# Kernel optimization log

Measured on AMD Instinct MI355X. Metric: run time of the kernel, lower is better.

## Reference

```python
import jax, jax.numpy as jnp
import numpy as np
from jax import lax

EPS = 1e-12


def _l2norm(v):
    return v / (jnp.sqrt(jnp.sum(v * v)) + EPS)


def _spectral_norm(W, u):
    # one torch-style power iteration; u, v are treated as constants
    v = lax.stop_gradient(_l2norm(W.T @ u))
    u2 = lax.stop_gradient(_l2norm(W @ v))
    sigma = u2 @ (W @ v)
    return W / sigma


def _lstm(gates_x, Whh):
    # gates_x: [B, T, 4H] = x @ Wih^T + b_ih + b_hh, precomputed
    B, T, G = gates_x.shape
    H = G // 4
    WhhT = Whh.T  # [H, 4H]

    def step(carry, gx_t):
        h, c = carry
        gates = gx_t + h @ WhhT  # [B, 4H]
        i = jax.nn.sigmoid(gates[:, 0 * H:1 * H])
        f = jax.nn.sigmoid(gates[:, 1 * H:2 * H])
        g = jnp.tanh(gates[:, 2 * H:3 * H])
        o = jax.nn.sigmoid(gates[:, 3 * H:4 * H])
        c = f * c + i * g
        h = o * jnp.tanh(c)
        return (h, c), h

    h0 = jnp.zeros((B, H), gates_x.dtype)
    c0 = jnp.zeros((B, H), gates_x.dtype)
    _, hs = lax.scan(step, (h0, c0), jnp.swapaxes(gates_x, 0, 1))
    return jnp.swapaxes(hs, 0, 1)  # [B, T, H]


def setup_inputs() -> dict:
    key = jax.random.key(0)
    ks = jax.random.split(key, 8)
    B, T, C, H = 512, 512, 32, 128
    Cin = C + 1  # minibatch-std channel
    init = lambda k, shp: 0.02 * jax.random.normal(k, shp, dtype=jnp.float32)
    return {
        "x": jax.random.normal(ks[0], (B, T, C), dtype=jnp.float32),
        "w_ih_orig": init(ks[1], (4 * H, Cin)),
        "u_ih": _l2norm(jax.random.normal(ks[2], (4 * H,), dtype=jnp.float32)),
        "w_hh_orig": init(ks[3], (4 * H, H)),
        "u_hh": _l2norm(jax.random.normal(ks[4], (4 * H,), dtype=jnp.float32)),
        "b_ih": jnp.zeros((4 * H,), jnp.float32),
        "b_hh": jnp.zeros((4 * H,), jnp.float32),
        "attn_w": init(ks[5], (1, H)),
        "attn_b": jnp.zeros((1,), jnp.float32),
        "fc_w_orig": init(ks[6], (1, H)),
        "u_fc": _l2norm(jax.random.normal(ks[7], (1,), dtype=jnp.float32)),
        "fc_b": jnp.zeros((1,), jnp.float32),
    }


def reference(x, w_ih_orig, u_ih, w_hh_orig, u_hh, b_ih, b_hh,
              attn_w, attn_b, fc_w_orig, u_fc, fc_b):
    B = x.shape[0]
    # minibatch std feature (torch std: unbiased, ddof=1)
    std_per_step = jnp.std(x, axis=0, ddof=1, keepdims=True)        # [1,T,C]
    std_scalar = jnp.mean(std_per_step, axis=-1, keepdims=True)     # [1,T,1]
    std_channel = jnp.broadcast_to(std_scalar, (B,) + std_scalar.shape[1:])
    x = jnp.concatenate([x, std_channel], axis=-1)                  # [B,T,C+1]

    Wih = _spectral_norm(w_ih_orig, u_ih)
    Whh = _spectral_norm(w_hh_orig, u_hh)
    gates_x = jnp.einsum("btc,gc->btg", x, Wih) + b_ih + b_hh       # [B,T,4H]
    h = _lstm(gates_x, Whh)                                          # [B,T,H]

    attn_logits = jnp.einsum("bth,oh->bto", h, attn_w) + attn_b     # [B,T,1]
    attn = jax.nn.softmax(attn_logits, axis=1)
    pooled = jnp.sum(attn * h, axis=1)                               # [B,H]

    Wfc = _spectral_norm(fc_w_orig, u_fc)
    score = pooled @ Wfc.T + fc_b                                    # [B,1]
    return score
```

## Files before the change

kernel.cpp:

```cpp
#include <hip/hip_runtime.h>
#include <math.h>

#define TT 512
#define BB 512
#define CC 32
#define CIN 33
#define HH 128
#define EPSF 1e-12f
#define CH 16
#define NCH (TT / CH)
#define RB 2
#define HSP 160
#define XSP 96

typedef _Float16 half8 __attribute__((ext_vector_type(8)));
typedef _Float16 half4v __attribute__((ext_vector_type(4)));
typedef _Float16 half2v __attribute__((ext_vector_type(2)));
typedef float f32x4 __attribute__((ext_vector_type(4)));

#define MFMA16H(a, b, c) __builtin_amdgcn_mfma_f32_16x16x32_f16(a, b, c, 0, 0, 0)

__device__ __forceinline__ float fsig(float x) {
    return __builtin_amdgcn_rcpf(1.f + __expf(-x));
}
__device__ __forceinline__ float ftanh(float x) {
    return 1.f - 2.f * __builtin_amdgcn_rcpf(1.f + __expf(2.f * x));
}
__device__ __forceinline__ float wave_sum_dpp(float x) {
    x += __int_as_float(__builtin_amdgcn_update_dpp(0, __float_as_int(x), 0x111, 0xf, 0xf, true));
    x += __int_as_float(__builtin_amdgcn_update_dpp(0, __float_as_int(x), 0x112, 0xf, 0xf, true));
    x += __int_as_float(__builtin_amdgcn_update_dpp(0, __float_as_int(x), 0x114, 0xf, 0xf, true));
    x += __int_as_float(__builtin_amdgcn_update_dpp(0, __float_as_int(x), 0x118, 0xf, 0xf, true));
    x += __int_as_float(__builtin_amdgcn_update_dpp(0, __float_as_int(x), 0x142, 0xa, 0xf, true));
    x += __int_as_float(__builtin_amdgcn_update_dpp(0, __float_as_int(x), 0x143, 0xc, 0xf, true));
    return x;
}
__device__ __forceinline__ float row_sum_dpp(float x) {
    x += __int_as_float(__builtin_amdgcn_update_dpp(0, __float_as_int(x), 0x111, 0xf, 0xf, true));
    x += __int_as_float(__builtin_amdgcn_update_dpp(0, __float_as_int(x), 0x112, 0xf, 0xf, true));
    x += __int_as_float(__builtin_amdgcn_update_dpp(0, __float_as_int(x), 0x114, 0xf, 0xf, true));
    x += __int_as_float(__builtin_amdgcn_update_dpp(0, __float_as_int(x), 0x118, 0xf, 0xf, true));
    return x;
}
__device__ __forceinline__ float load_s(const float* p) {
    float v = __hip_atomic_load(p, __ATOMIC_RELAXED, __HIP_MEMORY_SCOPE_AGENT);
    for (int it = 0; it < 100000000 && __float_as_uint(v) == 0xAAAAAAAAu; ++it)
        v = __hip_atomic_load(p, __ATOMIC_RELAXED, __HIP_MEMORY_SCOPE_AGENT);
    return v;
}

__global__ __attribute__((amdgpu_flat_work_group_size(512, 512), amdgpu_waves_per_eu(2, 2)))
void critic_fused(
    const float* __restrict__ x,
    const float* __restrict__ w_ih, const float* __restrict__ u_ih,
    const float* __restrict__ w_hh, const float* __restrict__ u_hh,
    const float* __restrict__ b_ih, const float* __restrict__ b_hh,
    const float* __restrict__ attn_w, const float* __restrict__ attn_b,
    const float* __restrict__ fc_w, const float* __restrict__ u_fc,
    const float* __restrict__ fc_b,
    float* __restrict__ ws,
    float* __restrict__ out)
{
    const int tid = threadIdx.x;
    const int w   = tid >> 6;
    const int l   = tid & 63;
    const int m   = l & 15;
    const int q   = l >> 4;
    const int r   = q & 1;
    const int b0  = blockIdx.x * RB;
    const int jcol = 16 * w + m;

    __shared__ float4 sSS[2][8][8];
    __shared__ float4 sQQ[2][8][8];
    __shared__ float stdp[2][8];
    __shared__ float red[512];
    __shared__ float vv[128];
    __shared__ float sigS[3];
    __shared__ __align__(16) _Float16 hs[2][RB][HSP];
    __shared__ __align__(16) _Float16 xs[2][CH][RB][XSP];
    __shared__ float ss[2][CH];
    __shared__ __align__(8) float bcast[2][RB];
    __shared__ float Sf[RB];
    __shared__ float part[8][RB];

    const int c4 = tid & 7;
    const int bs = tid >> 3;
    float4 xa[2][8];
#pragma unroll
    for (int tt = 0; tt < 2; ++tt) {
        const int t = 2 * blockIdx.x + tt;
#pragma unroll
        for (int i = 0; i < 8; ++i)
            xa[tt][i] = *reinterpret_cast<const float4*>(
                x + ((size_t)(bs * 8 + i) * TT + t) * CC + c4 * 4);
    }

    {
        const int c = tid & 127, qq = tid >> 7;
        const float* wp = w_hh + (size_t)(qq * 128) * HH + c;
        const float* up = u_hh + qq * 128;
        float a0 = 0.f, a1 = 0.f, a2 = 0.f, a3 = 0.f;
#pragma unroll 4
        for (int g = 0; g < 128; g += 4) {
            a0 = fmaf(wp[(size_t)(g + 0) * HH], up[g + 0], a0);
            a1 = fmaf(wp[(size_t)(g + 1) * HH], up[g + 1], a1);
            a2 = fmaf(wp[(size_t)(g + 2) * HH], up[g + 2], a2);
            a3 = fmaf(wp[(size_t)(g + 3) * HH], up[g + 3], a3);
        }
        red[tid] = (a0 + a1) + (a2 + a3);
    }

#pragma unroll
    for (int tt = 0; tt < 2; ++tt) {
        float4 S = make_float4(0.f, 0.f, 0.f, 0.f);
        float4 Q = make_float4(0.f, 0.f, 0.f, 0.f);
#pragma unroll
        for (int i = 0; i < 8; ++i) {
            float4 v = xa[tt][i];
            S.x += v.x; S.y += v.y; S.z += v.z; S.w += v.w;
            Q.x = fmaf(v.x, v.x, Q.x); Q.y = fmaf(v.y, v.y, Q.y);
            Q.z = fmaf(v.z, v.z, Q.z); Q.w = fmaf(v.w, v.w, Q.w);
        }
#pragma unroll
        for (int off = 8; off <= 32; off <<= 1) {
            S.x += __shfl_xor(S.x, off, 64); S.y += __shfl_xor(S.y, off, 64);
            S.z += __shfl_xor(S.z, off, 64); S.w += __shfl_xor(S.w, off, 64);
            Q.x += __shfl_xor(Q.x, off, 64); Q.y += __shfl_xor(Q.y, off, 64);
            Q.z += __shfl_xor(Q.z, off, 64); Q.w += __shfl_xor(Q.w, off, 64);
        }
        if (l < 8) { sSS[tt][w][c4] = S; sQQ[tt][w][c4] = Q; }
    }
    __syncthreads();

    if (tid < 128) vv[tid] = red[tid] + red[tid + 128] + red[tid + 256] + red[tid + 384];
    if (tid >= 384 && tid < 400) {
        const int tt2 = (tid - 384) >> 3, cc = (tid - 384) & 7;
        float4 St = make_float4(0.f, 0.f, 0.f, 0.f);
        float4 Qt = make_float4(0.f, 0.f, 0.f, 0.f);
#pragma unroll
        for (int i = 0; i < 8; ++i) {
            float4 a = sSS[tt2][i][cc], b4 = sQQ[tt2][i][cc];
            St.x += a.x; St.y += a.y; St.z += a.z; St.w += a.w;
            Qt.x += b4.x; Qt.y += b4.y; Qt.z += b4.z; Qt.w += b4.w;
        }
        float st = 0.f;
#pragma unroll
        for (int i = 0; i < 4; ++i) {
            float s1 = (i == 0) ? St.x : (i == 1) ? St.y : (i == 2) ? St.z : St.w;
            float q1 = (i == 0) ? Qt.x : (i == 1) ? Qt.y : (i == 2) ? Qt.z : Qt.w;
            float mean = s1 / 512.0f;
            float var  = (q1 - 512.0f * mean * mean) / 511.0f;
            st += sqrtf(fmaxf(var, 0.f));
        }
        stdp[tt2][cc] = st;
    }
    __syncthreads();
    if (tid >= 408 && tid < 410) {
        const int tt2 = tid - 408;
        float mm = 0.f;
#pragma unroll
        for (int i = 0; i < 8; ++i) mm += stdp[tt2][i];
        __hip_atomic_store(&ws[2 * blockIdx.x + tt2], mm / 32.0f, __ATOMIC_RELAXED,
                           __HIP_MEMORY_SCOPE_AGENT);
    }
    red[tid] = (tid < 128) ? vv[tid] * vv[tid] : 0.f;
    __syncthreads();

    {
        for (int s = 64; s >= 1; s >>= 1) { if (tid < s) red[tid] += red[tid + s]; __syncthreads(); }
        const float nv = sqrtf(red[0]);
        __syncthreads();
        if (tid < 128) vv[tid] = vv[tid] / (nv + EPSF);
        __syncthreads();
        float sq = 0.f;
        float2 vl = *reinterpret_cast<const float2*>(&vv[2 * l]);
#pragma unroll 4
        for (int gi = 0; gi < 64; ++gi) {
            const int g = w * 64 + gi;
            float2 wl = *reinterpret_cast<const float2*>(&w_hh[(size_t)g * HH + 2 * l]);
            float p  = fmaf(wl.x, vl.x, wl.y * vl.y);
            float tot = wave_sum_dpp(p);
            sq = fmaf(tot, tot, sq);
        }
        if (l == 63) red[w] = sq;
        __syncthreads();
        if (tid == 0) {
            float ns2 = 0.f;
            for (int i = 0; i < 8; ++i) ns2 += red[i];
            sigS[1] = ns2 / (sqrtf(ns2) + EPSF);
        }
        __syncthreads();
    }
    {
        if (l < CIN) {
            float a0 = 0.f, a1 = 0.f;
#pragma unroll 4
            for (int gi = 0; gi < 64; gi += 2) {
                const int g = w * 64 + gi;
                a0 = fmaf(w_ih[(size_t)(g + 0) * CIN + l], u_ih[g + 0], a0);
                a1 = fmaf(w_ih[(size_t)(g + 1) * CIN + l], u_ih[g + 1], a1);
            }
            red[w * 64 + l] = a0 + a1;
        }
        __syncthreads();
        if (tid < CIN) {
            float v = 0.f;
#pragma unroll
            for (int i = 0; i < 8; ++i) v += red[i * 64 + tid];
            vv[tid] = v;
        }
        __syncthreads();
        if (tid == 0) {
            float n2 = 0.f;
            for (int i = 0; i < CIN; ++i) n2 += vv[i] * vv[i];
            red[400] = sqrtf(n2);
        }
        __syncthreads();
        const float nv = red[400];
        if (tid < CIN) vv[tid] = vv[tid] / (nv + EPSF);
        __syncthreads();
        float vl = (l < CIN) ? vv[l] : 0.f;
        float sq = 0.f;
#pragma unroll 4
        for (int gi = 0; gi < 64; ++gi) {
            const int g = w * 64 + gi;
            float p = (l < CIN) ? w_ih[(size_t)g * CIN + l] * vl : 0.f;
            float tot = wave_sum_dpp(p);
            sq = fmaf(tot, tot, sq);
        }
        if (l == 63) red[w] = sq;
        __syncthreads();
        if (tid == 0) {
            float ns2 = 0.f;
            for (int i = 0; i < 8; ++i) ns2 += red[i];
            sigS[0] = ns2 / (sqrtf(ns2) + EPSF);
        }
        __syncthreads();
    }
    {
        red[tid] = (tid < 128) ? fc_w[tid] * fc_w[tid] : 0.f;
        __syncthreads();
        for (int s = 64; s >= 1; s >>= 1) { if (tid < s) red[tid] += red[tid + s]; __syncthreads(); }
        if (tid == 0) {
            float nw2 = red[0];
            float u0  = u_fc[0];
            float nv  = fabsf(u0) * sqrtf(nw2);
            float wv  = u0 * nw2 / (nv + EPSF);
            sigS[2]   = wv * wv / (fabsf(wv) + EPSF);
        }
        __syncthreads();
    }
    const float rih = 1.f / sigS[0];
    const float rhh = 1.f / sigS[1];
    const float rfc = 1.f / sigS[2];
    const float attb = attn_b[0];

    half8 Bf[4][5];
    float biasg[4], w32g[4];
#pragma unroll
    for (int p = 0; p < 4; ++p) {
        const int g = 16 * w + 128 * p + m;
#pragma unroll
        for (int kt = 0; kt < 4; ++kt) {
            const float* src = w_hh + (size_t)g * HH + kt * 32 + q * 8;
#pragma unroll
            for (int i = 0; i < 8; ++i) Bf[p][kt][i] = (_Float16)(src[i] * rhh);
        }
        {
            const float* src = w_ih + (size_t)g * CIN + q * 8;
#pragma unroll
            for (int i = 0; i < 8; ++i) Bf[p][4][i] = (_Float16)(src[i] * rih);
        }
        w32g[p]  = w_ih[(size_t)g * CIN + 32] * rih;
        biasg[p] = b_ih[g] + b_hh[g];
    }
    f32x4 zero4 = (f32x4){0.f, 0.f, 0.f, 0.f};
#pragma unroll
    for (int p = 0; p < 4; ++p) {
#pragma unroll
        for (int kt = 0; kt < 5; ++kt) asm volatile("" : "+v"(Bf[p][kt]));
        asm volatile("" : "+v"(biasg[p]), "+v"(w32g[p]));
    }
    asm volatile("" : "+v"(zero4));
    const float fcwj = fc_w[jcol] * rfc;
    const float aw0 = attn_w[2 * l];
    const float aw1 = attn_w[2 * l + 1];

    for (int i = tid; i < 2 * RB * HSP; i += 512) (&hs[0][0][0])[i] = (_Float16)0.f;
    if (tid < 256) {
        const int cc4 = tid & 7, rr = (tid >> 3) & 1, k = tid >> 4;
        float4 xv = *reinterpret_cast<const float4*>(x + ((size_t)(b0 + rr) * TT + k) * CC + cc4 * 4);
        half4v hv = {(_Float16)xv.x, (_Float16)xv.y, (_Float16)xv.z, (_Float16)xv.w};
        *(half4v*)&xs[0][k][rr][cc4 * 4] = hv;
    }
    if (tid < CH) ss[0][tid] = load_s(&ws[tid]);

    float c_st = 0.f, P = 0.f, hprev = 0.f, hpp = 0.f;
    float Sreg = 0.f;
    __syncthreads();

    for (int tc = 0; tc < NCH; ++tc) {
        const int cb = tc & 1;

        if (tc + 1 < NCH) {
            const int nb  = (tc + 1) & 1;
            const int t0n = (tc + 1) * CH;
            if (tid < 256) {
                const int cc4 = tid & 7, rr = (tid >> 3) & 1, k = tid >> 4;
                float4 xv = *reinterpret_cast<const float4*>(
                    x + ((size_t)(b0 + rr) * TT + (t0n + k)) * CC + cc4 * 4);
                half4v hv = {(_Float16)xv.x, (_Float16)xv.y, (_Float16)xv.z, (_Float16)xv.w};
                *(half4v*)&xs[nb][k][rr][cc4 * 4] = hv;
            }
            if (tid < CH) ss[nb][tid] = load_s(&ws[t0n + tid]);
        }

        for (int k = 0; k < CH; ++k) {
            const int t  = tc * CH + k;
            const int hb = (t + 1) & 1;

            half8 ah0 = *(const half8*)&hs[hb][m & 1][0 * 32 + q * 8];
            half8 ah1 = *(const half8*)&hs[hb][m & 1][1 * 32 + q * 8];
            half8 ah2 = *(const half8*)&hs[hb][m & 1][2 * 32 + q * 8];
            half8 ah3 = *(const half8*)&hs[hb][m & 1][3 * 32 + q * 8];
            half8 ah4 = *(const half8*)&xs[cb][k][m & 1][q * 8];
            const float s_t = ss[cb][k];

            float dotp = 0.f;
            if (t > 0 && w < RB) {
                half2v hh = *(const half2v*)&hs[hb][w][2 * l];
                dotp = fmaf(aw0, (float)hh[0], aw1 * (float)hh[1]);
            }

            if (t >= 2) P = fmaf(bcast[(t - 1) & 1][r], hpp, P);

            f32x4 acc0 = MFMA16H(ah0, Bf[0][0], zero4);
            f32x4 acc1 = MFMA16H(ah0, Bf[1][0], zero4);
            f32x4 acc2 = MFMA16H(ah0, Bf[2][0], zero4);
            f32x4 acc3 = MFMA16H(ah0, Bf[3][0], zero4);
            acc0 = MFMA16H(ah1, Bf[0][1], acc0);
            acc1 = MFMA16H(ah1, Bf[1][1], acc1);
            acc2 = MFMA16H(ah1, Bf[2][1], acc2);
            acc3 = MFMA16H(ah1, Bf[3][1], acc3);
            acc0 = MFMA16H(ah2, Bf[0][2], acc0);
            acc1 = MFMA16H(ah2, Bf[1][2], acc1);
            acc2 = MFMA16H(ah2, Bf[2][2], acc2);
            acc3 = MFMA16H(ah2, Bf[3][2], acc3);
            acc0 = MFMA16H(ah3, Bf[0][3], acc0);
            acc1 = MFMA16H(ah3, Bf[1][3], acc1);
            acc2 = MFMA16H(ah3, Bf[2][3], acc2);
            acc3 = MFMA16H(ah3, Bf[3][3], acc3);
            acc0 = MFMA16H(ah4, Bf[0][4], acc0);
            acc1 = MFMA16H(ah4, Bf[1][4], acc1);
            acc2 = MFMA16H(ah4, Bf[2][4], acc2);
            acc3 = MFMA16H(ah4, Bf[3][4], acc3);

            if (t > 0 && w < RB) {
                float tot = wave_sum_dpp(dotp);
                if (l == 63) {
                    float beta = __expf(tot + attb);
                    Sreg += beta;
                    bcast[t & 1][w] = beta;
                }
            }

            {
                float g0 = acc0[r] + fmaf(w32g[0], s_t, biasg[0]);
                float g1 = acc1[r] + fmaf(w32g[1], s_t, biasg[1]);
                float g2 = acc2[r] + fmaf(w32g[2], s_t, biasg[2]);
                float g3 = acc3[r] + fmaf(w32g[3], s_t, biasg[3]);
                float ig = fsig(g0);
                float fg = fsig(g1);
                float gg = ftanh(g2);
                float og = fsig(g3);
                c_st = fmaf(fg, c_st, ig * gg);
                float hv = og * ftanh(c_st);
                hpp   = hprev;
                hprev = hv;
                if (q < 2) hs[t & 1][r][jcol] = (_Float16)hv;
            }

            __syncthreads();
        }
    }

    P = fmaf(bcast[1][r], hpp, P);
    if (w < RB) {
        half2v hh = *(const half2v*)&hs[1][w][2 * l];
        float dotp = fmaf(aw0, (float)hh[0], aw1 * (float)hh[1]);
        float tot = wave_sum_dpp(dotp);
        if (l == 63) {
            float beta = __expf(tot + attb);
            Sreg += beta;
            bcast[0][w] = beta;
            Sf[w] = Sreg;
        }
    }
    __syncthreads();
    {
        float Pv = fmaf(bcast[0][r], hprev, P);
        float v  = Pv * __builtin_amdgcn_rcpf(Sf[r]) * fcwj;
        float rs = row_sum_dpp(v);
        if (l == 15) part[w][0] = rs;
        if (l == 31) part[w][1] = rs;
    }
    __syncthreads();
    if (tid < RB) {
        float a = 0.f;
#pragma unroll
        for (int i = 0; i < 8; ++i) a += part[i][tid];
        out[b0 + tid] = a + fc_b[0];
    }
}

extern "C" void kernel_launch(void* const* d_in, const int* in_sizes, int n_in,
                              void* d_out, int out_size, void* d_ws, size_t ws_size,
                              hipStream_t stream) {
    const float* x      = (const float*)d_in[0];
    const float* w_ih   = (const float*)d_in[1];
    const float* u_ih   = (const float*)d_in[2];
    const float* w_hh   = (const float*)d_in[3];
    const float* u_hh   = (const float*)d_in[4];
    const float* b_ih   = (const float*)d_in[5];
    const float* b_hh   = (const float*)d_in[6];
    const float* attn_w = (const float*)d_in[7];
    const float* attn_b = (const float*)d_in[8];
    const float* fc_w   = (const float*)d_in[9];
    const float* u_fc   = (const float*)d_in[10];
    const float* fc_b   = (const float*)d_in[11];
    float* ws  = (float*)d_ws;
    float* out = (float*)d_out;

    critic_fused<<<BB / RB, 512, 0, stream>>>(x, w_ih, u_ih, w_hh, u_hh, b_ih, b_hh,
                                              attn_w, attn_b, fc_w, u_fc, fc_b, ws, out);
}
```

Baseline: 467.4 us.

## Precompute input-gate projections per chunk via MFMA, off the recurrent critical path

The x-projection MFMA (fifth K-slice) leaves the per-step recurrent chain. Instead, the next chunk's gate pre-activations, including the std-channel term and biases, are computed in bulk with MFMAs partway through the current chunk and stored as fp32 in shared memory. Each step then does 16 MFMAs plus four LDS loads. The change also swaps __syncthreads for a raw lgkmcnt wait plus s_barrier, and moves the attention waves to waves 6-7. The cost is a much larger LDS footprint (about 130KB) and extra LDS traffic.

```diff
diff --git a/kernel.cpp b/kernel.cpp
--- a/kernel.cpp
+++ b/kernel.cpp
@@ -11,14 +11,14 @@
 #define NCH (TT / CH)
 #define RB 2
 #define HSP 160
-#define XSP 96
+#define GXP 520
 
 typedef _Float16 half8 __attribute__((ext_vector_type(8)));
-typedef _Float16 half4v __attribute__((ext_vector_type(4)));
 typedef _Float16 half2v __attribute__((ext_vector_type(2)));
 typedef float f32x4 __attribute__((ext_vector_type(4)));
 
 #define MFMA16H(a, b, c) __builtin_amdgcn_mfma_f32_16x16x32_f16(a, b, c, 0, 0, 0)
+#define BARRIER() asm volatile("s_waitcnt lgkmcnt(0)\n\ts_barrier" ::: "memory")
 
 __device__ __forceinline__ float fsig(float x) {
     return __builtin_amdgcn_rcpf(1.f + __expf(-x));
@@ -77,8 +77,7 @@
     __shared__ float vv[128];
     __shared__ float sigS[3];
     __shared__ __align__(16) _Float16 hs[2][RB][HSP];
-    __shared__ __align__(16) _Float16 xs[2][CH][RB][XSP];
-    __shared__ float ss[2][CH];
+    __shared__ float gxs[2][2 * CH][GXP];
     __shared__ __align__(8) float bcast[2][RB];
     __shared__ float Sf[RB];
     __shared__ float part[8][RB];
@@ -286,114 +285,139 @@
     const float aw0 = attn_w[2 * l];
     const float aw1 = attn_w[2 * l + 1];
 
+#define STAGE_LOAD(t0_, xr_)                                                   \
+    {                                                                          \
+        _Pragma("unroll")                                                      \
+        for (int mt = 0; mt < 2; ++mt) {                                       \
+            const size_t base =                                                \
+                ((size_t)(b0 + (m & 1)) * TT + ((t0_) + 8 * mt + (m >> 1))) *  \
+                    CC + q * 8;                                                \
+            xr_[mt][0] = *reinterpret_cast<const float4*>(x + base);           \
+            xr_[mt][1] = *reinterpret_cast<const float4*>(x + base + 4);       \
+        }                                                                      \
+    }
+
+#define STAGE_COMMIT(t0_, nb_, xr_)                                            \
+    {                                                                          \
+        _Pragma("unroll")                                                      \
+        for (int mt = 0; mt < 2; ++mt) {                                       \
+            half8 af = {(_Float16)xr_[mt][0].x, (_Float16)xr_[mt][0].y,        \
+                        (_Float16)xr_[mt][0].z, (_Float16)xr_[mt][0].w,        \
+                        (_Float16)xr_[mt][1].x, (_Float16)xr_[mt][1].y,        \
+                        (_Float16)xr_[mt][1].z, (_Float16)xr_[mt][1].w};       \
+            f32x4 s0 = MFMA16H(af, Bf[0][4], zero4);                           \
+            f32x4 s1 = MFMA16H(af, Bf[1][4], zero4);                           \
+            f32x4 s2 = MFMA16H(af, Bf[2][4], zero4);                           \
+            f32x4 s3 = MFMA16H(af, Bf[3][4], zero4);                           \
+            const float svl = load_s(&ws[(t0_) + 8 * mt + 2 * q]);             \
+            const float svh = load_s(&ws[(t0_) + 8 * mt + 2 * q + 1]);         \
+            const int row0 = 16 * mt + 4 * q;                                  \
+            _Pragma("unroll")                                                  \
+            for (int j = 0; j < 4; ++j) {                                      \
+                const float sv = (j & 2) ? svh : svl;                          \
+                gxs[nb_][row0 + j][jcol + 0]   = s0[j] + fmaf(w32g[0], sv, biasg[0]); \
+                gxs[nb_][row0 + j][jcol + 128] = s1[j] + fmaf(w32g[1], sv, biasg[1]); \
+                gxs[nb_][row0 + j][jcol + 256] = s2[j] + fmaf(w32g[2], sv, biasg[2]); \
+                gxs[nb_][row0 + j][jcol + 384] = s3[j] + fmaf(w32g[3], sv, biasg[3]); \
+            }                                                                  \
+        }                                                                      \
+    }
+
+#define LSTM_STEP(t_, k_, cb_)                                                 \
+    {                                                                          \
+        const int t  = (t_);                                                   \
+        const int hb = (t + 1) & 1;                                            \
+        half8 ah0 = *(const half8*)&hs[hb][m & 1][0 * 32 + q * 8];             \
+        half8 ah1 = *(const half8*)&hs[hb][m & 1][1 * 32 + q * 8];             \
+        half8 ah2 = *(const half8*)&hs[hb][m & 1][2 * 32 + q * 8];             \
+        half8 ah3 = *(const half8*)&hs[hb][m & 1][3 * 32 + q * 8];             \
+        const float* gxr = &gxs[cb_][((k_) << 1) | r][jcol];                   \
+        float gx0 = gxr[0];                                                    \
+        float gx1 = gxr[128];                                                  \
+        float gx2 = gxr[256];                                                  \
+        float gx3 = gxr[384];                                                  \
+        float dotp = 0.f;                                                      \
+        if (t > 0 && w >= 6) {                                                 \
+            half2v hh = *(const half2v*)&hs[hb][w - 6][2 * l];                 \
+            dotp = fmaf(aw0, (float)hh[0], aw1 * (float)hh[1]);                \
+        }                                                                      \
+        if (t >= 2) P = fmaf(bcast[(t - 1) & 1][r], hpp, P);                   \
+        f32x4 acc0 = MFMA16H(ah0, Bf[0][0], zero4);                            \
+        f32x4 acc1 = MFMA16H(ah0, Bf[1][0], zero4);                            \
+        f32x4 acc2 = MFMA16H(ah0, Bf[2][0], zero4);                            \
+        f32x4 acc3 = MFMA16H(ah0, Bf[3][0], zero4);                            \
+        acc0 = MFMA16H(ah1, Bf[0][1], acc0);                                   \
+        acc1 = MFMA16H(ah1, Bf[1][1], acc1);                                   \
+        acc2 = MFMA16H(ah1, Bf[2][1], acc2);                                   \
+        acc3 = MFMA16H(ah1, Bf[3][1], acc3);                                   \
+        acc0 = MFMA16H(ah2, Bf[0][2], acc0);                                   \
+        acc1 = MFMA16H(ah2, Bf[1][2], acc1);                                   \
+        acc2 = MFMA16H(ah2, Bf[2][2], acc2);                                   \
+        acc3 = MFMA16H(ah2, Bf[3][2], acc3);                                   \
+        acc0 = MFMA16H(ah3, Bf[0][3], acc0);                                   \
+        acc1 = MFMA16H(ah3, Bf[1][3], acc1);                                   \
+        acc2 = MFMA16H(ah3, Bf[2][3], acc2);                                   \
+        acc3 = MFMA16H(ah3, Bf[3][3], acc3);                                   \
+        if (t > 0 && w >= 6) {                                                 \
+            float tot = wave_sum_dpp(dotp);                                    \
+            if (l == 63) {                                                     \
+                float beta = __expf(tot + attb);                               \
+                Sreg += beta;                                                  \
+                bcast[t & 1][w - 6] = beta;                                    \
+            }                                                                  \
+        }                                                                      \
+        {                                                                      \
+            float g0 = acc0[r] + gx0;                                          \
+            float g1 = acc1[r] + gx1;                                          \
+            float g2 = acc2[r] + gx2;                                          \
+            float g3 = acc3[r] + gx3;                                          \
+            float ig = fsig(g0);                                               \
+            float fg = fsig(g1);                                               \
+            float gg = ftanh(g2);                                              \
+            float og = fsig(g3);                                               \
+            c_st = fmaf(fg, c_st, ig * gg);                                    \
+            float hv = og * ftanh(c_st);                                       \
+            hpp   = hprev;                                                     \
+            hprev = hv;                                                        \
+            if (q < 2) hs[t & 1][r][jcol] = (_Float16)hv;                      \
+        }                                                                      \
+        BARRIER();                                                             \
+    }
+
     for (int i = tid; i < 2 * RB * HSP; i += 512) (&hs[0][0][0])[i] = (_Float16)0.f;
-    if (tid < 256) {
-        const int cc4 = tid & 7, rr = (tid >> 3) & 1, k = tid >> 4;
-        float4 xv = *reinterpret_cast<const float4*>(x + ((size_t)(b0 + rr) * TT + k) * CC + cc4 * 4);
-        half4v hv = {(_Float16)xv.x, (_Float16)xv.y, (_Float16)xv.z, (_Float16)xv.w};
-        *(half4v*)&xs[0][k][rr][cc4 * 4] = hv;
-    }
-    if (tid < CH) ss[0][tid] = load_s(&ws[tid]);
 
     float c_st = 0.f, P = 0.f, hprev = 0.f, hpp = 0.f;
     float Sreg = 0.f;
+
+    {
+        float4 xr0[2][2];
+        STAGE_LOAD(0, xr0);
+        STAGE_COMMIT(0, 0, xr0);
+    }
     __syncthreads();
 
     for (int tc = 0; tc < NCH; ++tc) {
-        const int cb = tc & 1;
-
-        if (tc + 1 < NCH) {
-            const int nb  = (tc + 1) & 1;
-            const int t0n = (tc + 1) * CH;
-            if (tid < 256) {
-                const int cc4 = tid & 7, rr = (tid >> 3) & 1, k = tid >> 4;
-                float4 xv = *reinterpret_cast<const float4*>(
-                    x + ((size_t)(b0 + rr) * TT + (t0n + k)) * CC + cc4 * 4);
-                half4v hv = {(_Float16)xv.x, (_Float16)xv.y, (_Float16)xv.z, (_Float16)xv.w};
-                *(half4v*)&xs[nb][k][rr][cc4 * 4] = hv;
-            }
-            if (tid < CH) ss[nb][tid] = load_s(&ws[t0n + tid]);
-        }
-
-        for (int k = 0; k < CH; ++k) {
-            const int t  = tc * CH + k;
-            const int hb = (t + 1) & 1;
-
-            half8 ah0 = *(const half8*)&hs[hb][m & 1][0 * 32 + q * 8];
-            half8 ah1 = *(const half8*)&hs[hb][m & 1][1 * 32 + q * 8];
-            half8 ah2 = *(const half8*)&hs[hb][m & 1][2 * 32 + q * 8];
-            half8 ah3 = *(const half8*)&hs[hb][m & 1][3 * 32 + q * 8];
-            half8 ah4 = *(const half8*)&xs[cb][k][m & 1][q * 8];
-            const float s_t = ss[cb][k];
-
-            float dotp = 0.f;
-            if (t > 0 && w < RB) {
-                half2v hh = *(const half2v*)&hs[hb][w][2 * l];
-                dotp = fmaf(aw0, (float)hh[0], aw1 * (float)hh[1]);
-            }
-
-            if (t >= 2) P = fmaf(bcast[(t - 1) & 1][r], hpp, P);
-
-            f32x4 acc0 = MFMA16H(ah0, Bf[0][0], zero4);
-            f32x4 acc1 = MFMA16H(ah0, Bf[1][0], zero4);
-            f32x4 acc2 = MFMA16H(ah0, Bf[2][0], zero4);
-            f32x4 acc3 = MFMA16H(ah0, Bf[3][0], zero4);
-            acc0 = MFMA16H(ah1, Bf[0][1], acc0);
-            acc1 = MFMA16H(ah1, Bf[1][1], acc1);
-            acc2 = MFMA16H(ah1, Bf[2][1], acc2);
-            acc3 = MFMA16H(ah1, Bf[3][1], acc3);
-            acc0 = MFMA16H(ah2, Bf[0][2], acc0);
-            acc1 = MFMA16H(ah2, Bf[1][2], acc1);
-            acc2 = MFMA16H(ah2, Bf[2][2], acc2);
-            acc3 = MFMA16H(ah2, Bf[3][2], acc3);
-            acc0 = MFMA16H(ah3, Bf[0][3], acc0);
-            acc1 = MFMA16H(ah3, Bf[1][3], acc1);
-            acc2 = MFMA16H(ah3, Bf[2][3], acc2);
-            acc3 = MFMA16H(ah3, Bf[3][3], acc3);
-            acc0 = MFMA16H(ah4, Bf[0][4], acc0);
-            acc1 = MFMA16H(ah4, Bf[1][4], acc1);
-            acc2 = MFMA16H(ah4, Bf[2][4], acc2);
-            acc3 = MFMA16H(ah4, Bf[3][4], acc3);
-
-            if (t > 0 && w < RB) {
-                float tot = wave_sum_dpp(dotp);
-                if (l == 63) {
-                    float beta = __expf(tot + attb);
-                    Sreg += beta;
-                    bcast[t & 1][w] = beta;
-                }
-            }
-
-            {
-                float g0 = acc0[r] + fmaf(w32g[0], s_t, biasg[0]);
-                float g1 = acc1[r] + fmaf(w32g[1], s_t, biasg[1]);
-                float g2 = acc2[r] + fmaf(w32g[2], s_t, biasg[2]);
-                float g3 = acc3[r] + fmaf(w32g[3], s_t, biasg[3]);
-                float ig = fsig(g0);
-                float fg = fsig(g1);
-                float gg = ftanh(g2);
-                float og = fsig(g3);
-                c_st = fmaf(fg, c_st, ig * gg);
-                float hv = og * ftanh(c_st);
-                hpp   = hprev;
-                hprev = hv;
-                if (q < 2) hs[t & 1][r][jcol] = (_Float16)hv;
-            }
-
-            __syncthreads();
-        }
+        const int cb  = tc & 1;
+        const int t0n = (tc + 1) * CH;
+        float4 xr[2][2];
+        if (tc + 1 < NCH) STAGE_LOAD(t0n, xr);
+#pragma unroll 2
+        for (int k = 0; k < CH / 2; ++k) LSTM_STEP(tc * CH + k, k, cb);
+        if (tc + 1 < NCH) STAGE_COMMIT(t0n, cb ^ 1, xr);
+#pragma unroll 2
+        for (int k = CH / 2; k < CH; ++k) LSTM_STEP(tc * CH + k, k, cb);
     }
 
     P = fmaf(bcast[1][r], hpp, P);
-    if (w < RB) {
-        half2v hh = *(const half2v*)&hs[1][w][2 * l];
+    if (w >= 6) {
+        half2v hh = *(const half2v*)&hs[1][w - 6][2 * l];
         float dotp = fmaf(aw0, (float)hh[0], aw1 * (float)hh[1]);
         float tot = wave_sum_dpp(dotp);
         if (l == 63) {
             float beta = __expf(tot + attb);
             Sreg += beta;
-            bcast[0][w] = beta;
-            Sf[w] = Sreg;
+            bcast[0][w - 6] = beta;
+            Sf[w - 6] = Sreg;
         }
     }
     __syncthreads();
```

Result: no change. 471.7 us (+0.9%).

## Specialize waves: 4 for recurrence MFMAs, 4 for input-gate precompute and attention

Applied to the files above, without the earlier changes.

Splits the 8 waves into two roles. Four waves run the recurrent h·Whh MFMAs, each now covering 32 hidden columns with all gate lanes active. The other four precompute the input projection x·Wih plus bias and the std term for the next chunk into shared memory in fp32, spread across steps, and also handle the attention logits. This takes the input-projection MFMA off the serial critical path and replaces __syncthreads with a raw barrier. In exchange the recurrent waves do twice the MFMAs per step and shared memory use grows with the fp32 gate buffer.

```diff
diff --git a/kernel.cpp b/kernel.cpp
--- a/kernel.cpp
+++ b/kernel.cpp
@@ -11,14 +11,14 @@
 #define NCH (TT / CH)
 #define RB 2
 #define HSP 160
-#define XSP 96
+#define GXP 520
 
 typedef _Float16 half8 __attribute__((ext_vector_type(8)));
-typedef _Float16 half4v __attribute__((ext_vector_type(4)));
 typedef _Float16 half2v __attribute__((ext_vector_type(2)));
 typedef float f32x4 __attribute__((ext_vector_type(4)));
 
 #define MFMA16H(a, b, c) __builtin_amdgcn_mfma_f32_16x16x32_f16(a, b, c, 0, 0, 0)
+#define BARRIER() asm volatile("s_waitcnt lgkmcnt(0)\n\ts_barrier" ::: "memory")
 
 __device__ __forceinline__ float fsig(float x) {
     return __builtin_amdgcn_rcpf(1.f + __expf(-x));
@@ -66,9 +66,11 @@
     const int l   = tid & 63;
     const int m   = l & 15;
     const int q   = l >> 4;
-    const int r   = q & 1;
     const int b0  = blockIdx.x * RB;
-    const int jcol = 16 * w + m;
+    const int sw  = w - 4;
+    const int col = 32 * (w & 3) + (l & 31);
+    const int row = l >> 5;
+    const int sub = (l >> 4) & 1;
 
     __shared__ float4 sSS[2][8][8];
     __shared__ float4 sQQ[2][8][8];
@@ -77,11 +79,10 @@
     __shared__ float vv[128];
     __shared__ float sigS[3];
     __shared__ __align__(16) _Float16 hs[2][RB][HSP];
-    __shared__ __align__(16) _Float16 xs[2][CH][RB][XSP];
-    __shared__ float ss[2][CH];
+    __shared__ __align__(16) float gxs[2][CH][RB][GXP];
     __shared__ __align__(8) float bcast[2][RB];
     __shared__ float Sf[RB];
-    __shared__ float part[8][RB];
+    __shared__ float part[4][4];
 
     const int c4 = tid & 7;
     const int bs = tid >> 3;
@@ -255,120 +256,163 @@
     const float rfc = 1.f / sigS[2];
     const float attb = attn_b[0];
 
-    half8 Bf[4][5];
-    float biasg[4], w32g[4];
-#pragma unroll
-    for (int p = 0; p < 4; ++p) {
-        const int g = 16 * w + 128 * p + m;
-#pragma unroll
-        for (int kt = 0; kt < 4; ++kt) {
-            const float* src = w_hh + (size_t)g * HH + kt * 32 + q * 8;
-#pragma unroll
-            for (int i = 0; i < 8; ++i) Bf[p][kt][i] = (_Float16)(src[i] * rhh);
-        }
-        {
-            const float* src = w_ih + (size_t)g * CIN + q * 8;
-#pragma unroll
-            for (int i = 0; i < 8; ++i) Bf[p][4][i] = (_Float16)(src[i] * rih);
-        }
-        w32g[p]  = w_ih[(size_t)g * CIN + 32] * rih;
-        biasg[p] = b_ih[g] + b_hh[g];
-    }
+    half8 BREG[4][2][4];
+    float biasg[4][2], w32g[4][2];
+    float fcwj = 0.f, aw0 = 0.f, aw1 = 0.f;
     f32x4 zero4 = (f32x4){0.f, 0.f, 0.f, 0.f};
-#pragma unroll
-    for (int p = 0; p < 4; ++p) {
-#pragma unroll
-        for (int kt = 0; kt < 5; ++kt) asm volatile("" : "+v"(Bf[p][kt]));
-        asm volatile("" : "+v"(biasg[p]), "+v"(w32g[p]));
+    if (w < 4) {
+#pragma unroll
+        for (int p = 0; p < 4; ++p)
+#pragma unroll
+            for (int s = 0; s < 2; ++s) {
+                const int g = 128 * p + 32 * w + 16 * s + m;
+#pragma unroll
+                for (int kt = 0; kt < 4; ++kt) {
+                    const float* src = w_hh + (size_t)g * HH + kt * 32 + q * 8;
+#pragma unroll
+                    for (int i = 0; i < 8; ++i) BREG[p][s][kt][i] = (_Float16)(src[i] * rhh);
+                }
+            }
+#pragma unroll
+        for (int p = 0; p < 4; ++p)
+#pragma unroll
+            for (int s = 0; s < 2; ++s)
+#pragma unroll
+                for (int kt = 0; kt < 4; ++kt) asm volatile("" : "+v"(BREG[p][s][kt]));
+        fcwj = fc_w[col] * rfc;
+    } else {
+#pragma unroll
+        for (int p = 0; p < 4; ++p)
+#pragma unroll
+            for (int s = 0; s < 2; ++s) {
+                const int g = 128 * p + 32 * sw + 16 * s + m;
+                const float* src = w_ih + (size_t)g * CIN + q * 8;
+#pragma unroll
+                for (int i = 0; i < 8; ++i) BREG[p][s][0][i] = (_Float16)(src[i] * rih);
+                w32g[p][s]  = w_ih[(size_t)g * CIN + 32] * rih;
+                biasg[p][s] = b_ih[g] + b_hh[g];
+                asm volatile("" : "+v"(BREG[p][s][0]));
+                asm volatile("" : "+v"(biasg[p][s]), "+v"(w32g[p][s]));
+            }
+        aw0 = attn_w[2 * l];
+        aw1 = attn_w[2 * l + 1];
     }
     asm volatile("" : "+v"(zero4));
-    const float fcwj = fc_w[jcol] * rfc;
-    const float aw0 = attn_w[2 * l];
-    const float aw1 = attn_w[2 * l + 1];
+
+#define STAGE_LOAD(t0_, xr_)                                                   \
+    {                                                                          \
+        _Pragma("unroll")                                                      \
+        for (int mt = 0; mt < 2; ++mt) {                                       \
+            const size_t base =                                                \
+                ((size_t)(b0 + (m & 1)) * TT + ((t0_) + 8 * mt + (m >> 1))) *  \
+                    CC + q * 8;                                                \
+            xr_[mt][0] = *reinterpret_cast<const float4*>(x + base);           \
+            xr_[mt][1] = *reinterpret_cast<const float4*>(x + base + 4);       \
+        }                                                                      \
+    }
+
+#define STAGE_SPIN(t0_, svr_)                                                  \
+    {                                                                          \
+        svr_[0] = load_s(&ws[(t0_) + 2 * q]);                                  \
+        svr_[1] = load_s(&ws[(t0_) + 2 * q + 1]);                              \
+        svr_[2] = load_s(&ws[(t0_) + 8 + 2 * q]);                              \
+        svr_[3] = load_s(&ws[(t0_) + 8 + 2 * q + 1]);                          \
+    }
+
+#define STAGE_COMMIT(nb_, xr_, svr_)                                           \
+    {                                                                          \
+        _Pragma("unroll")                                                      \
+        for (int mt = 0; mt < 2; ++mt) {                                       \
+            half8 af = {(_Float16)xr_[mt][0].x, (_Float16)xr_[mt][0].y,        \
+                        (_Float16)xr_[mt][0].z, (_Float16)xr_[mt][0].w,        \
+                        (_Float16)xr_[mt][1].x, (_Float16)xr_[mt][1].y,        \
+                        (_Float16)xr_[mt][1].z, (_Float16)xr_[mt][1].w};       \
+            _Pragma("unroll")                                                  \
+            for (int s = 0; s < 2; ++s) {                                      \
+                f32x4 s0 = MFMA16H(af, BREG[0][s][0], zero4);                  \
+                f32x4 s1 = MFMA16H(af, BREG[1][s][0], zero4);                  \
+                f32x4 s2 = MFMA16H(af, BREG[2][s][0], zero4);                  \
+                f32x4 s3 = MFMA16H(af, BREG[3][s][0], zero4);                  \
+                _Pragma("unroll")                                              \
+                for (int j = 0; j < 4; ++j) {                                  \
+                    const float sv = (j & 2) ? svr_[2 * mt + 1] : svr_[2 * mt];\
+                    f32x4 gv;                                                  \
+                    gv[0] = s0[j] + fmaf(w32g[0][s], sv, biasg[0][s]);         \
+                    gv[1] = s1[j] + fmaf(w32g[1][s], sv, biasg[1][s]);         \
+                    gv[2] = s2[j] + fmaf(w32g[2][s], sv, biasg[2][s]);         \
+                    gv[3] = s3[j] + fmaf(w32g[3][s], sv, biasg[3][s]);         \
+                    *reinterpret_cast<f32x4*>(                                 \
+                        &gxs[nb_][8 * mt + 2 * q + (j >> 1)][j & 1]            \
+                            [(32 * sw + 16 * s + m) * 4]) = gv;                \
+                }                                                              \
+            }                                                                  \
+        }                                                                      \
+    }
 
     for (int i = tid; i < 2 * RB * HSP; i += 512) (&hs[0][0][0])[i] = (_Float16)0.f;
-    if (tid < 256) {
-        const int cc4 = tid & 7, rr = (tid >> 3) & 1, k = tid >> 4;
-        float4 xv = *reinterpret_cast<const float4*>(x + ((size_t)(b0 + rr) * TT + k) * CC + cc4 * 4);
-        half4v hv = {(_Float16)xv.x, (_Float16)xv.y, (_Float16)xv.z, (_Float16)xv.w};
-        *(half4v*)&xs[0][k][rr][cc4 * 4] = hv;
-    }
-    if (tid < CH) ss[0][tid] = load_s(&ws[tid]);
 
     float c_st = 0.f, P = 0.f, hprev = 0.f, hpp = 0.f;
     float Sreg = 0.f;
+    float4 xr[2][2];
+    float svr[4];
+
+    if (w >= 4) {
+        STAGE_LOAD(0, xr);
+        STAGE_SPIN(0, svr);
+        STAGE_COMMIT(0, xr, svr);
+    }
     __syncthreads();
 
     for (int tc = 0; tc < NCH; ++tc) {
-        const int cb = tc & 1;
-
-        if (tc + 1 < NCH) {
-            const int nb  = (tc + 1) & 1;
-            const int t0n = (tc + 1) * CH;
-            if (tid < 256) {
-                const int cc4 = tid & 7, rr = (tid >> 3) & 1, k = tid >> 4;
-                float4 xv = *reinterpret_cast<const float4*>(
-                    x + ((size_t)(b0 + rr) * TT + (t0n + k)) * CC + cc4 * 4);
-                half4v hv = {(_Float16)xv.x, (_Float16)xv.y, (_Float16)xv.z, (_Float16)xv.w};
-                *(half4v*)&xs[nb][k][rr][cc4 * 4] = hv;
-            }
-            if (tid < CH) ss[nb][tid] = load_s(&ws[t0n + tid]);
-        }
-
+        const int cb  = tc & 1;
+        const int t0n = (tc + 1) * CH;
+#pragma unroll 2
         for (int k = 0; k < CH; ++k) {
             const int t  = tc * CH + k;
             const int hb = (t + 1) & 1;
-
-            half8 ah0 = *(const half8*)&hs[hb][m & 1][0 * 32 + q * 8];
-            half8 ah1 = *(const half8*)&hs[hb][m & 1][1 * 32 + q * 8];
-            half8 ah2 = *(const half8*)&hs[hb][m & 1][2 * 32 + q * 8];
-            half8 ah3 = *(const half8*)&hs[hb][m & 1][3 * 32 + q * 8];
-            half8 ah4 = *(const half8*)&xs[cb][k][m & 1][q * 8];
-            const float s_t = ss[cb][k];
-
-            float dotp = 0.f;
-            if (t > 0 && w < RB) {
-                half2v hh = *(const half2v*)&hs[hb][w][2 * l];
-                dotp = fmaf(aw0, (float)hh[0], aw1 * (float)hh[1]);
-            }
-
-            if (t >= 2) P = fmaf(bcast[(t - 1) & 1][r], hpp, P);
-
-            f32x4 acc0 = MFMA16H(ah0, Bf[0][0], zero4);
-            f32x4 acc1 = MFMA16H(ah0, Bf[1][0], zero4);
-            f32x4 acc2 = MFMA16H(ah0, Bf[2][0], zero4);
-            f32x4 acc3 = MFMA16H(ah0, Bf[3][0], zero4);
-            acc0 = MFMA16H(ah1, Bf[0][1], acc0);
-            acc1 = MFMA16H(ah1, Bf[1][1], acc1);
-            acc2 = MFMA16H(ah1, Bf[2][1], acc2);
-            acc3 = MFMA16H(ah1, Bf[3][1], acc3);
-            acc0 = MFMA16H(ah2, Bf[0][2], acc0);
-            acc1 = MFMA16H(ah2, Bf[1][2], acc1);
-            acc2 = MFMA16H(ah2, Bf[2][2], acc2);
-            acc3 = MFMA16H(ah2, Bf[3][2], acc3);
-            acc0 = MFMA16H(ah3, Bf[0][3], acc0);
-            acc1 = MFMA16H(ah3, Bf[1][3], acc1);
-            acc2 = MFMA16H(ah3, Bf[2][3], acc2);
-            acc3 = MFMA16H(ah3, Bf[3][3], acc3);
-            acc0 = MFMA16H(ah4, Bf[0][4], acc0);
-            acc1 = MFMA16H(ah4, Bf[1][4], acc1);
-            acc2 = MFMA16H(ah4, Bf[2][4], acc2);
-            acc3 = MFMA16H(ah4, Bf[3][4], acc3);
-
-            if (t > 0 && w < RB) {
-                float tot = wave_sum_dpp(dotp);
-                if (l == 63) {
-                    float beta = __expf(tot + attb);
-                    Sreg += beta;
-                    bcast[t & 1][w] = beta;
-                }
-            }
-
-            {
-                float g0 = acc0[r] + fmaf(w32g[0], s_t, biasg[0]);
-                float g1 = acc1[r] + fmaf(w32g[1], s_t, biasg[1]);
-                float g2 = acc2[r] + fmaf(w32g[2], s_t, biasg[2]);
-                float g3 = acc3[r] + fmaf(w32g[3], s_t, biasg[3]);
+            if (w < 4) {
+                half8 ah0 = *(const half8*)&hs[hb][m & 1][0 * 32 + q * 8];
+                half8 ah1 = *(const half8*)&hs[hb][m & 1][1 * 32 + q * 8];
+                half8 ah2 = *(const half8*)&hs[hb][m & 1][2 * 32 + q * 8];
+                half8 ah3 = *(const half8*)&hs[hb][m & 1][3 * 32 + q * 8];
+                f32x4 gx4 = *reinterpret_cast<const f32x4*>(&gxs[cb][k][row][col * 4]);
+                if (t >= 2) P = fmaf(bcast[(t - 1) & 1][row], hpp, P);
+                f32x4 c00 = MFMA16H(ah0, BREG[0][0][0], zero4);
+                f32x4 c10 = MFMA16H(ah0, BREG[0][1][0], zero4);
+                f32x4 c01 = MFMA16H(ah0, BREG[1][0][0], zero4);
+                f32x4 c11 = MFMA16H(ah0, BREG[1][1][0], zero4);
+                f32x4 c02 = MFMA16H(ah0, BREG[2][0][0], zero4);
+                f32x4 c12 = MFMA16H(ah0, BREG[2][1][0], zero4);
+                f32x4 c03 = MFMA16H(ah0, BREG[3][0][0], zero4);
+                f32x4 c13 = MFMA16H(ah0, BREG[3][1][0], zero4);
+                c00 = MFMA16H(ah1, BREG[0][0][1], c00);
+                c10 = MFMA16H(ah1, BREG[0][1][1], c10);
+                c01 = MFMA16H(ah1, BREG[1][0][1], c01);
+                c11 = MFMA16H(ah1, BREG[1][1][1], c11);
+                c02 = MFMA16H(ah1, BREG[2][0][1], c02);
+                c12 = MFMA16H(ah1, BREG[2][1][1], c12);
+                c03 = MFMA16H(ah1, BREG[3][0][1], c03);
+                c13 = MFMA16H(ah1, BREG[3][1][1], c13);
+                c00 = MFMA16H(ah2, BREG[0][0][2], c00);
+                c10 = MFMA16H(ah2, BREG[0][1][2], c10);
+                c01 = MFMA16H(ah2, BREG[1][0][2], c01);
+                c11 = MFMA16H(ah2, BREG[1][1][2], c11);
+                c02 = MFMA16H(ah2, BREG[2][0][2], c02);
+                c12 = MFMA16H(ah2, BREG[2][1][2], c12);
+                c03 = MFMA16H(ah2, BREG[3][0][2], c03);
+                c13 = MFMA16H(ah2, BREG[3][1][2], c13);
+                c00 = MFMA16H(ah3, BREG[0][0][3], c00);
+                c10 = MFMA16H(ah3, BREG[0][1][3], c10);
+                c01 = MFMA16H(ah3, BREG[1][0][3], c01);
+                c11 = MFMA16H(ah3, BREG[1][1][3], c11);
+                c02 = MFMA16H(ah3, BREG[2][0][3], c02);
+                c12 = MFMA16H(ah3, BREG[2][1][3], c12);
+                c03 = MFMA16H(ah3, BREG[3][0][3], c03);
+                c13 = MFMA16H(ah3, BREG[3][1][3], c13);
+                float g0 = (sub ? (row ? c10[1] : c10[0]) : (row ? c00[1] : c00[0])) + gx4[0];
+                float g1 = (sub ? (row ? c11[1] : c11[0]) : (row ? c01[1] : c01[0])) + gx4[1];
+                float g2 = (sub ? (row ? c12[1] : c12[0]) : (row ? c02[1] : c02[0])) + gx4[2];
+                float g3 = (sub ? (row ? c13[1] : c13[0]) : (row ? c03[1] : c03[0])) + gx4[3];
                 float ig = fsig(g0);
                 float fg = fsig(g1);
                 float gg = ftanh(g2);
@@ -377,38 +421,52 @@
                 float hv = og * ftanh(c_st);
                 hpp   = hprev;
                 hprev = hv;
-                if (q < 2) hs[t & 1][r][jcol] = (_Float16)hv;
+                hs[t & 1][row][col] = (_Float16)hv;
+            } else {
+                if (sw < 2 && t > 0) {
+                    half2v hh = *(const half2v*)&hs[hb][sw][2 * l];
+                    float dotp = fmaf(aw0, (float)hh[0], aw1 * (float)hh[1]);
+                    float tot = wave_sum_dpp(dotp);
+                    if (l == 63) {
+                        float beta = __expf(tot + attb);
+                        Sreg += beta;
+                        bcast[t & 1][sw] = beta;
+                    }
+                }
+                if (tc + 1 < NCH) {
+                    if (k == 0) STAGE_LOAD(t0n, xr);
+                    if (k == 4) STAGE_SPIN(t0n, svr);
+                    if (k == 8) STAGE_COMMIT(cb ^ 1, xr, svr);
+                }
             }
-
-            __syncthreads();
-        }
-    }
-
-    P = fmaf(bcast[1][r], hpp, P);
-    if (w < RB) {
-        half2v hh = *(const half2v*)&hs[1][w][2 * l];
+            BARRIER();
+        }
+    }
+
+    if (w < 4) P = fmaf(bcast[1][row], hpp, P);
+    if (w >= 4 && sw < 2) {
+        half2v hh = *(const half2v*)&hs[1][sw][2 * l];
         float dotp = fmaf(aw0, (float)hh[0], aw1 * (float)hh[1]);
         float tot = wave_sum_dpp(dotp);
         if (l == 63) {
             float beta = __expf(tot + attb);
             Sreg += beta;
-            bcast[0][w] = beta;
-            Sf[w] = Sreg;
-        }
-    }
-    __syncthreads();
-    {
-        float Pv = fmaf(bcast[0][r], hprev, P);
-        float v  = Pv * __builtin_amdgcn_rcpf(Sf[r]) * fcwj;
+            bcast[0][sw] = beta;
+            Sf[sw] = Sreg;
+        }
+    }
+    __syncthreads();
+    if (w < 4) {
+        float Pv = fmaf(bcast[0][row], hprev, P);
+        float v  = Pv * __builtin_amdgcn_rcpf(Sf[row]) * fcwj;
         float rs = row_sum_dpp(v);
-        if (l == 15) part[w][0] = rs;
-        if (l == 31) part[w][1] = rs;
+        if ((l & 15) == 15) part[w][q] = rs;
     }
     __syncthreads();
     if (tid < RB) {
         float a = 0.f;
 #pragma unroll
-        for (int i = 0; i < 8; ++i) a += part[i][tid];
+        for (int i = 0; i < 4; ++i) a += part[i][2 * tid] + part[i][2 * tid + 1];
         out[b0 + tid] = a + fc_b[0];
     }
 }
```

New measurement: 390.2 us. -16.5%, faster.
